# Performance work log

Hardware: AMD Instinct MI355X
Metric: run time of the kernel (lower is better)

The kernel has to match this reference:

```python
import jax, jax.numpy as jnp
import numpy as np

IOU_THRESHOLD = 0.5
ROIS_NUMBER = 256


def setup_inputs() -> dict:
    key = jax.random.key(0)
    k1, k2, k3 = jax.random.split(key, 3)
    B, N = 8, 4096
    scores = jax.random.uniform(k1, (B, N, 1), dtype=jnp.float32)
    xy = jax.random.uniform(k2, (B, N, 2), dtype=jnp.float32) * 100.0
    wh = jax.random.uniform(k3, (B, N, 2), dtype=jnp.float32) * 20.0 + 1.0
    return {"input": jnp.concatenate([scores, xy, wh], axis=-1)}


def _make_corners(regs):
    # regs: [N,4] = (x, y, w, h); TF uses floor-div by 2 (`//`) on floats
    x, y, w, h = regs[:, 0], regs[:, 1], regs[:, 2], regs[:, 3]
    ws = w // 2
    hs = h // 2
    return jnp.stack([x - ws, y - hs, x + ws, y + hs], axis=-1)


def _nms_single(preds, key):
    # preds: [N,5] = (score, x, y, w, h)
    N = preds.shape[0]
    scores = preds[:, 0]
    boxes = _make_corners(preds[:, 1:])
    order = jnp.argsort(-scores)                       # descending score
    b = boxes[order]
    x1, y1, x2, y2 = b[:, 0], b[:, 1], b[:, 2], b[:, 3]
    area = (x2 - x1) * (y2 - y1)
    # pairwise IoU [N,N] (selection only -> stop_gradient)
    ix1 = jnp.maximum(x1[:, None], x1[None, :])
    iy1 = jnp.maximum(y1[:, None], y1[None, :])
    ix2 = jnp.minimum(x2[:, None], x2[None, :])
    iy2 = jnp.minimum(y2[:, None], y2[None, :])
    inter = jnp.maximum(ix2 - ix1, 0.0) * jnp.maximum(iy2 - iy1, 0.0)
    union = area[:, None] + area[None, :] - inter
    iou = jax.lax.stop_gradient(jnp.where(union > 0, inter / union, 0.0))

    idx = jnp.arange(N)

    def step(suppressed, i):
        keep_i = ~suppressed[i]
        suppressed = suppressed | (keep_i & (iou[i] > IOU_THRESHOLD) & (idx > i))
        return suppressed, keep_i

    _, keep = jax.lax.scan(step, jnp.zeros((N,), bool), idx)

    # first ROIS_NUMBER kept positions (in score order); N marks "not kept"
    pos = jnp.sort(jnp.where(keep, idx, N))[:ROIS_NUMBER]
    valid = pos < N
    sel = order[jnp.minimum(pos, N - 1)]
    rand_idx = jax.random.randint(key, (ROIS_NUMBER,), 0, N)
    sel = jnp.where(valid, sel, rand_idx)              # pad with random regions
    return preds[sel][:, 1:]                           # [ROIS,4] = (x,y,w,h)


def reference(input) -> jnp.ndarray:
    B = input.shape[0]
    keys = jax.random.split(jax.random.key(42), B)
    return jax.vmap(_nms_single)(input, keys)
```

## Files before the change

### kernel.cpp

```cpp
#include <hip/hip_runtime.h>
#include <stdint.h>

#pragma clang fp contract(off)

#define NMS_B 8
#define NMS_N 4096
#define ROIS 256
#define SEL_TAU 0.85f

typedef unsigned long long u64;
typedef unsigned int u32;

__device__ __forceinline__ int lds_slot(int e) { return e + (e >> 2); }

__device__ __forceinline__ u64 rdlane_u64(u64 v, int l) {
    u32 lo = (u32)__builtin_amdgcn_readlane((int)(u32)v, l);
    u32 hi = (u32)__builtin_amdgcn_readlane((int)(u32)(v >> 32), l);
    return ((u64)hi << 32) | lo;
}

__device__ __forceinline__ bool sup_pred(float4 rc, float rh, float4 cc, float ch) {
    float iw = fmaxf(fminf(rc.z, cc.z) - fmaxf(rc.x, cc.x), 0.0f);
    float ih = fmaxf(fminf(rc.w, cc.w) - fmaxf(rc.y, cc.y), 0.0f);
    float inter = iw * ih;
    return inter > fmaf(-0.5f, inter, rh + ch);
}


__global__ __launch_bounds__(1024, 1) void nms_k1(
        const float* __restrict__ in, float4* __restrict__ crn512,
        float* __restrict__ ha512, u32* __restrict__ sidx512,
        int* __restrict__ flag) {
    __shared__ u64 sm[3584];
    __shared__ int s_selCount;
    const int b = blockIdx.x, t = threadIdx.x;
    const int lane = t & 63;
    const size_t base = (size_t)b * NMS_N;

    u64* selKey = sm;
    u64* sortA0 = sm + 1024;
    u64* sortA1 = sm + 2304;

    float sc[4];
    #pragma unroll
    for (int r = 0; r < 4; ++r) {
        int e = t + 1024 * r;
        sc[r] = in[(base + e) * 5];
    }
    if (t == 0) s_selCount = 0;
    __syncthreads();

    #pragma unroll
    for (int r = 0; r < 4; ++r) {
        bool pred = (sc[r] >= SEL_TAU);
        u64 m = __ballot(pred);
        u32 cnt = (u32)__popcll(m);
        int wbase = 0;
        if (lane == 0 && cnt) wbase = atomicAdd(&s_selCount, (int)cnt);
        wbase = __shfl(wbase, 0, 64);
        if (pred) {
            int slot = wbase + (int)__popcll(m & ((1ULL << lane) - 1ULL));
            if (slot < 1024) {
                int e = t + 1024 * r;
                selKey[slot] = ((u64)(~__float_as_uint(sc[r])) << 32) | (u32)e;
            }
        }
    }
    __syncthreads();
    const int selCount = s_selCount;
    const bool fullPath = (selCount < 512) || (selCount > 1024);
    if (t == 0) flag[b] = fullPath ? 1 : 0;
    if (fullPath) return;

    u64 kk = (t < selCount) ? selKey[t] : ~0ULL;
    int s = 0;
    for (int k = 2; k <= 1024; k <<= 1) {
        int j = k >> 1;
        for (; j >= 64; j >>= 1) {
            u64* buf = s ? sortA1 : sortA0;
            buf[lds_slot(t)] = kk;
            __syncthreads();
            u64 part = buf[lds_slot(t ^ j)];
            bool up = ((t & k) == 0), lower = ((t & j) == 0);
            u64 mn = kk < part ? kk : part, mx = kk < part ? part : kk;
            kk = (up == lower) ? mn : mx;
            s ^= 1;
        }
        for (; j >= 1; j >>= 1) {
            u64 part = __shfl_xor(kk, j, 64);
            bool up = ((t & k) == 0), lower = ((t & j) == 0);
            u64 mn = kk < part ? kk : part, mx = kk < part ? part : kk;
            kk = (up == lower) ? mn : mx;
        }
    }

    if (t < 512) {
        u32 orig = (u32)kk;
        const float* bp = in + (base + orig) * 5;
        float x = bp[1], y = bp[2], w = bp[3], h = bp[4];
        float ws_ = floorf(w * 0.5f), hs_ = floorf(h * 0.5f);
        float4 c4 = make_float4(x - ws_, y - hs_, x + ws_, y + hs_);
        size_t g = (size_t)b * 512 + t;
        crn512[g] = c4;
        ha512[g] = 0.5f * ((c4.z - c4.x) * (c4.w - c4.y));
        sidx512[g] = orig;
    }
}

__global__ __launch_bounds__(256, 1) void nms_k2(
        const float4* __restrict__ crn512, const float* __restrict__ ha512,
        const int* __restrict__ flag, u64* __restrict__ hbuf) {
    const int b = blockIdx.y, blk = blockIdx.x;
    if (flag[b]) return;
    __shared__ float4 crn_s[512];
    __shared__ float  ha_s[512];
    const int t = threadIdx.x, lane = t & 63, wid = t >> 6;

    for (int i = t; i < 512; i += 256) {
        crn_s[i] = crn512[(size_t)b * 512 + i];
        ha_s[i]  = ha512[(size_t)b * 512 + i];
    }
    __syncthreads();

    u32* h32 = (u32*)hbuf;
    #pragma unroll
    for (int s = 0; s < 2; ++s) {
        int tau = blk * 8 + wid * 2 + s;
        int u = tau >> 1, hf = tau & 1;
        int kr = 0;
        while ((kr + 1) * (kr + 2) / 2 <= u) ++kr;
        int w = u - kr * (kr + 1) / 2;
        float4 myc = crn_s[64 * kr + lane];
        float  myh = ha_s[64 * kr + lane];
        u32 word = 0;
        const int q0 = hf * 32;
        #pragma unroll 8
        for (int q = 0; q < 32; ++q) {
            bool p = sup_pred(crn_s[64 * w + q0 + q], ha_s[64 * w + q0 + q], myc, myh);
            word |= (u32)(p ? 1u : 0u) << q;
        }
        h32[(((size_t)b * 36 + u) * 64 + lane) * 2 + hf] = word;
    }
}

__global__ __launch_bounds__(1024, 1) void nms_k3(
        const float* __restrict__ in, const u32* __restrict__ sidx512,
        const u64* __restrict__ hbuf, const int* __restrict__ flag,
        u32* __restrict__ sortedIdx, float4* __restrict__ crn,
        float* __restrict__ ha, float* __restrict__ outp) {
    __shared__ u64 sm[5120];
    __shared__ int kept[ROIS];
    __shared__ int s_need;
    const int b = blockIdx.x, t = threadIdx.x;
    const int lane = t & 63, wid = t >> 6;
    const size_t base = (size_t)b * NMS_N;

    int flg = flag[b];
    if (!flg) {
        for (int i = t; i < 2304; i += 1024) sm[i] = hbuf[(size_t)b * 2304 + i];
        for (int r = t; r < ROIS; r += 1024) kept[r] = 0;
        if (t == 0) s_need = 0;
        __syncthreads();

        if (t < 64) {
            u64* h_lds = sm;
            int count = 0;
            u32 f[8];
            #pragma unroll
            for (int k = 0; k < 8; ++k) f[k] = 1u;
            bool done = false;
            #pragma unroll
            for (int g = 0; g < 8; ++g) {
                if (!done) {
                    u64 hgg = h_lds[(g * (g + 1) / 2 + g) * 64 + lane];
                    u64 kb = 0;
                    u64 avail = __ballot(f[g] != 0);
                    while (avail != 0 && count < ROIS) {
                        int r = __builtin_ctzll(avail);
                        if (lane == 0) kept[count] = g * 64 + r;
                        ++count;
                        kb |= 1ULL << r;
                        u64 w = rdlane_u64(hgg, r);
                        avail &= ~(w | (1ULL << r));
                    }
                    if (count >= ROIS) {
                        done = true;
                    } else {
                        #pragma unroll
                        for (int k2 = g + 1; k2 < 8; ++k2)
                            f[k2] &= (u32)((h_lds[(k2 * (k2 + 1) / 2 + g) * 64 + lane] & kb) == 0);
                    }
                }
            }
            if (t == 0) s_need = (count >= ROIS) ? 0 : 1;
        }
        __syncthreads();
        flg = s_need;
    }

    if (flg) {
        u64 key[4];
        #pragma unroll
        for (int r = 0; r < 4; ++r) {
            int e = 4 * t + r;
            float s = in[(base + e) * 5];
            key[r] = ((u64)(~__float_as_uint(s)) << 32) | (u32)e;
        }
        for (int k = 2; k <= 4096; k <<= 1) {
            int j = k >> 1;
            if (j >= 256) {
                #pragma unroll
                for (int r = 0; r < 4; ++r) sm[lds_slot(4 * t + r)] = key[r];
                __syncthreads();
                for (; j >= 256; j >>= 1) {
                    for (int el = t; el < 4096; el += 1024) {
                        int p = el ^ j;
                        if (p > el) {
                            u64 a = sm[lds_slot(el)], cc = sm[lds_slot(p)];
                            bool up = ((el & k) == 0);
                            if ((a > cc) == up) { sm[lds_slot(el)] = cc; sm[lds_slot(p)] = a; }
                        }
                    }
                    __syncthreads();
                }
                #pragma unroll
                for (int r = 0; r < 4; ++r) key[r] = sm[lds_slot(4 * t + r)];
            }
            for (; j >= 4; j >>= 1) {
                int d = j >> 2;
                #pragma unroll
                for (int r = 0; r < 4; ++r) {
                    int e = 4 * t + r;
                    u64 mine = key[r];
                    u64 part = __shfl_xor(mine, d, 64);
                    bool up = ((e & k) == 0);
                    bool lower = ((e & j) == 0);
                    u64 mn = (mine < part) ? mine : part;
                    u64 mx = (mine < part) ? part : mine;
                    key[r] = (up == lower) ? mn : mx;
                }
            }
            for (; j >= 1; j >>= 1) {
                #pragma unroll
                for (int r = 0; r < 4; ++r) {
                    int pr = r | j;
                    if (((r & j) == 0) && pr < 4) {
                        int e = 4 * t + r;
                        bool up = ((e & k) == 0);
                        u64 a = key[r], cc = key[pr];
                        if ((a > cc) == up) { key[r] = cc; key[pr] = a; }
                    }
                }
            }
        }
        __syncthreads();

        u64*    h2 = sm;
        float4* crn2 = (float4*)(sm + 2304);
        float*  ha2  = (float*)(sm + 2304 + 1024);

        #pragma unroll
        for (int r = 0; r < 4; ++r) {
            int e = 4 * t + r;
            u32 orig = (u32)key[r];
            const float* bp = in + (base + orig) * 5;
            float x = bp[1], y = bp[2], w = bp[3], h = bp[4];
            float ws_ = floorf(w * 0.5f), hs_ = floorf(h * 0.5f);
            float4 c4 = make_float4(x - ws_, y - hs_, x + ws_, y + hs_);
            float hv = 0.5f * ((c4.z - c4.x) * (c4.w - c4.y));
            size_t g = base + e;
            sortedIdx[g] = orig;
            crn[g] = c4;
            ha[g] = hv;
            if (e < 512) { crn2[e] = c4; ha2[e] = hv; }
        }
        for (int r = t; r < ROIS; r += 1024) kept[r] = 0;
        __syncthreads();

        for (int u = wid; u < 36; u += 16) {
            int kr = 0;
            while ((kr + 1) * (kr + 2) / 2 <= u) ++kr;
            int w = u - kr * (kr + 1) / 2;
            float4 myc = crn2[64 * kr + lane];
            float  myh = ha2[64 * kr + lane];
            u64 word = 0;
            #pragma unroll 4
            for (int q = 0; q < 64; ++q) {
                bool p = sup_pred(crn2[64 * w + q], ha2[64 * w + q], myc, myh);
                word |= ((u64)(p ? 1u : 0u)) << q;
            }
            h2[(size_t)u * 64 + lane] = word;
        }
        __syncthreads();

        if (t < 64) {
            int count = 0;
            u32 f[8];
            #pragma unroll
            for (int k = 0; k < 8; ++k) f[k] = 1u;
            bool done = false;
            #pragma unroll
            for (int g = 0; g < 8; ++g) {
                if (!done) {
                    u64 hgg = h2[(size_t)(g * (g + 1) / 2 + g) * 64 + lane];
                    u64 kb = 0;
                    u64 avail = __ballot(f[g] != 0);
                    while (avail != 0 && count < ROIS) {
                        int r = __builtin_ctzll(avail);
                        if (lane == 0) kept[count] = g * 64 + r;
                        ++count;
                        kb |= 1ULL << r;
                        u32 bit = (u32)(hgg >> r) & 1u;
                        f[g] &= (bit ^ 1u) & (u32)(lane != r);
                        avail = __ballot(f[g] != 0);
                    }
                    if (count >= ROIS) {
                        done = true;
                    } else {
                        #pragma unroll
                        for (int k2 = g + 1; k2 < 8; ++k2)
                            f[k2] &= (u32)((h2[(size_t)(k2 * (k2 + 1) / 2 + g) * 64 + lane] & kb) == 0);
                    }
                }
            }
            if (count < ROIS) {
                for (int Wp = 4; Wp < 32 && count < ROIS; ++Wp) {
                    const int cLo = 128 * Wp + lane, cHi = cLo + 64;
                    float4 cL = crn[base + cLo]; float hL = ha[base + cLo];
                    float4 cH = crn[base + cHi]; float hH = ha[base + cHi];
                    u32 fLo = 1u, fHi = 1u;
                    for (int j2 = 0; j2 < count; ++j2) {
                        int pos = kept[j2];
                        float4 kc = crn[base + pos]; float kh = ha[base + pos];
                        fLo &= (u32)(!sup_pred(kc, kh, cL, hL));
                        fHi &= (u32)(!sup_pred(kc, kh, cH, hH));
                    }
                    u64 curLo0 = 0, curHi0 = 0, curHi1 = 0;
                    for (int r = 0; r < 64; ++r) {
                        float4 rc = crn[base + 128 * Wp + r]; float rh = ha[base + 128 * Wp + r];
                        curLo0 |= ((u64)(sup_pred(rc, rh, cL, hL) ? 1u : 0u)) << r;
                        curHi0 |= ((u64)(sup_pred(rc, rh, cH, hH) ? 1u : 0u)) << r;
                    }
                    for (int r = 0; r < 64; ++r) {
                        float4 rc = crn[base + 128 * Wp + 64 + r]; float rh = ha[base + 128 * Wp + 64 + r];
                        curHi1 |= ((u64)(sup_pred(rc, rh, cH, hH) ? 1u : 0u)) << r;
                    }
                    u64 availLo = __ballot(fLo != 0);
                    while (availLo != 0 && count < ROIS) {
                        int r = __builtin_ctzll(availLo);
                        if (lane == 0) kept[count] = Wp * 128 + r;
                        ++count;
                        fLo &= (u32)(((curLo0 >> r) & 1ULL) ^ 1ULL) & (u32)(lane != r);
                        fHi &= (u32)(((curHi0 >> r) & 1ULL) ^ 1ULL);
                        availLo = __ballot(fLo != 0);
                    }
                    u64 availHi = __ballot(fHi != 0);
                    while (availHi != 0 && count < ROIS) {
                        int r = __builtin_ctzll(availHi);
                        if (lane == 0) kept[count] = Wp * 128 + 64 + r;
                        ++count;
                        fHi &= (u32)(((curHi1 >> r) & 1ULL) ^ 1ULL) & (u32)(lane != r);
                        availHi = __ballot(fHi != 0);
                    }
                }
            }
        }
    }
    __syncthreads();

    if (t < ROIS) {
        int pos = kept[t];
        int orig = flg ? (int)sortedIdx[base + pos]
                       : (int)sidx512[(size_t)b * 512 + pos];
        const float* bp = in + (base + orig) * 5;
        ((float4*)outp)[(size_t)b * ROIS + t] =
            make_float4(bp[1], bp[2], bp[3], bp[4]);
    }
}

extern "C" void kernel_launch(void* const* d_in, const int* in_sizes, int n_in,
                              void* d_out, int out_size, void* d_ws, size_t ws_size,
                              hipStream_t stream) {
    const float* in = (const float*)d_in[0];
    float* out = (float*)d_out;
    char* ws = (char*)d_ws;

    u32* sortedIdx = (u32*)ws;                  size_t off = (size_t)NMS_B * NMS_N * 4;
    float4* crn = (float4*)(ws + off);          off += (size_t)NMS_B * NMS_N * 16;
    float* ha = (float*)(ws + off);             off += (size_t)NMS_B * NMS_N * 4;
    float4* crn512 = (float4*)(ws + off);       off += (size_t)NMS_B * 512 * 16;
    float* ha512 = (float*)(ws + off);          off += (size_t)NMS_B * 512 * 4;
    u32* sidx512 = (u32*)(ws + off);            off += (size_t)NMS_B * 512 * 4;
    u64* hbuf = (u64*)(ws + off);               off += (size_t)NMS_B * 36 * 64 * 8;
    int* flag = (int*)(ws + off);               off += NMS_B * 4;

    nms_k1<<<NMS_B, 1024, 0, stream>>>(in, crn512, ha512, sidx512, flag);
    nms_k2<<<dim3(9, NMS_B), 256, 0, stream>>>(crn512, ha512, flag, hbuf);
    nms_k3<<<NMS_B, 1024, 0, stream>>>(in, sidx512, hbuf, flag, sortedIdx, crn, ha, out);
}
```

Before: 92.95 us.

## Move fast-path greedy scan into k2 via last-block atomic, full path into k1

The full-sort fallback path moves into k1. The fast-path greedy selection and output write move from k3 into k2, where the last-arriving block per batch (atomic counter with threadfences) runs the scan. k2 now launches twice as many blocks, each doing one word, and writes kept indices by popcount instead of serially. k3 becomes a rarely-taken recovery path gated by needFull. This removes the separate 1024-thread k3 pass and its hbuf reload on the common path, at the cost of atomic/fence overhead and duplicated code.

```diff
diff --git a/kernel.cpp b/kernel.cpp
--- a/kernel.cpp
+++ b/kernel.cpp
@@ -30,11 +30,14 @@
 __global__ __launch_bounds__(1024, 1) void nms_k1(
         const float* __restrict__ in, float4* __restrict__ crn512,
         float* __restrict__ ha512, u32* __restrict__ sidx512,
-        int* __restrict__ flag) {
-    __shared__ u64 sm[3584];
+        int* __restrict__ flag, int* __restrict__ done, int* __restrict__ needFull,
+        u32* __restrict__ sortedIdx, float4* __restrict__ crn,
+        float* __restrict__ ha, float* __restrict__ outp) {
+    __shared__ u64 sm[5120];
+    __shared__ int kept[ROIS];
     __shared__ int s_selCount;
     const int b = blockIdx.x, t = threadIdx.x;
-    const int lane = t & 63;
+    const int lane = t & 63, wid = t >> 6;
     const size_t base = (size_t)b * NMS_N;
 
     u64* selKey = sm;
@@ -47,7 +50,7 @@
         int e = t + 1024 * r;
         sc[r] = in[(base + e) * 5];
     }
-    if (t == 0) s_selCount = 0;
+    if (t == 0) { s_selCount = 0; done[b] = 0; needFull[b] = 0; }
     __syncthreads();
 
     #pragma unroll
@@ -70,135 +73,44 @@
     const int selCount = s_selCount;
     const bool fullPath = (selCount < 512) || (selCount > 1024);
     if (t == 0) flag[b] = fullPath ? 1 : 0;
-    if (fullPath) return;
-
-    u64 kk = (t < selCount) ? selKey[t] : ~0ULL;
-    int s = 0;
-    for (int k = 2; k <= 1024; k <<= 1) {
-        int j = k >> 1;
-        for (; j >= 64; j >>= 1) {
-            u64* buf = s ? sortA1 : sortA0;
-            buf[lds_slot(t)] = kk;
-            __syncthreads();
-            u64 part = buf[lds_slot(t ^ j)];
-            bool up = ((t & k) == 0), lower = ((t & j) == 0);
-            u64 mn = kk < part ? kk : part, mx = kk < part ? part : kk;
-            kk = (up == lower) ? mn : mx;
-            s ^= 1;
-        }
-        for (; j >= 1; j >>= 1) {
-            u64 part = __shfl_xor(kk, j, 64);
-            bool up = ((t & k) == 0), lower = ((t & j) == 0);
-            u64 mn = kk < part ? kk : part, mx = kk < part ? part : kk;
-            kk = (up == lower) ? mn : mx;
-        }
-    }
-
-    if (t < 512) {
-        u32 orig = (u32)kk;
-        const float* bp = in + (base + orig) * 5;
-        float x = bp[1], y = bp[2], w = bp[3], h = bp[4];
-        float ws_ = floorf(w * 0.5f), hs_ = floorf(h * 0.5f);
-        float4 c4 = make_float4(x - ws_, y - hs_, x + ws_, y + hs_);
-        size_t g = (size_t)b * 512 + t;
-        crn512[g] = c4;
-        ha512[g] = 0.5f * ((c4.z - c4.x) * (c4.w - c4.y));
-        sidx512[g] = orig;
-    }
-}
-
-__global__ __launch_bounds__(256, 1) void nms_k2(
-        const float4* __restrict__ crn512, const float* __restrict__ ha512,
-        const int* __restrict__ flag, u64* __restrict__ hbuf) {
-    const int b = blockIdx.y, blk = blockIdx.x;
-    if (flag[b]) return;
-    __shared__ float4 crn_s[512];
-    __shared__ float  ha_s[512];
-    const int t = threadIdx.x, lane = t & 63, wid = t >> 6;
-
-    for (int i = t; i < 512; i += 256) {
-        crn_s[i] = crn512[(size_t)b * 512 + i];
-        ha_s[i]  = ha512[(size_t)b * 512 + i];
-    }
-    __syncthreads();
-
-    u32* h32 = (u32*)hbuf;
-    #pragma unroll
-    for (int s = 0; s < 2; ++s) {
-        int tau = blk * 8 + wid * 2 + s;
-        int u = tau >> 1, hf = tau & 1;
-        int kr = 0;
-        while ((kr + 1) * (kr + 2) / 2 <= u) ++kr;
-        int w = u - kr * (kr + 1) / 2;
-        float4 myc = crn_s[64 * kr + lane];
-        float  myh = ha_s[64 * kr + lane];
-        u32 word = 0;
-        const int q0 = hf * 32;
-        #pragma unroll 8
-        for (int q = 0; q < 32; ++q) {
-            bool p = sup_pred(crn_s[64 * w + q0 + q], ha_s[64 * w + q0 + q], myc, myh);
-            word |= (u32)(p ? 1u : 0u) << q;
-        }
-        h32[(((size_t)b * 36 + u) * 64 + lane) * 2 + hf] = word;
-    }
-}
-
-__global__ __launch_bounds__(1024, 1) void nms_k3(
-        const float* __restrict__ in, const u32* __restrict__ sidx512,
-        const u64* __restrict__ hbuf, const int* __restrict__ flag,
-        u32* __restrict__ sortedIdx, float4* __restrict__ crn,
-        float* __restrict__ ha, float* __restrict__ outp) {
-    __shared__ u64 sm[5120];
-    __shared__ int kept[ROIS];
-    __shared__ int s_need;
-    const int b = blockIdx.x, t = threadIdx.x;
-    const int lane = t & 63, wid = t >> 6;
-    const size_t base = (size_t)b * NMS_N;
-
-    int flg = flag[b];
-    if (!flg) {
-        for (int i = t; i < 2304; i += 1024) sm[i] = hbuf[(size_t)b * 2304 + i];
-        for (int r = t; r < ROIS; r += 1024) kept[r] = 0;
-        if (t == 0) s_need = 0;
-        __syncthreads();
-
-        if (t < 64) {
-            u64* h_lds = sm;
-            int count = 0;
-            u32 f[8];
-            #pragma unroll
-            for (int k = 0; k < 8; ++k) f[k] = 1u;
-            bool done = false;
-            #pragma unroll
-            for (int g = 0; g < 8; ++g) {
-                if (!done) {
-                    u64 hgg = h_lds[(g * (g + 1) / 2 + g) * 64 + lane];
-                    u64 kb = 0;
-                    u64 avail = __ballot(f[g] != 0);
-                    while (avail != 0 && count < ROIS) {
-                        int r = __builtin_ctzll(avail);
-                        if (lane == 0) kept[count] = g * 64 + r;
-                        ++count;
-                        kb |= 1ULL << r;
-                        u64 w = rdlane_u64(hgg, r);
-                        avail &= ~(w | (1ULL << r));
-                    }
-                    if (count >= ROIS) {
-                        done = true;
-                    } else {
-                        #pragma unroll
-                        for (int k2 = g + 1; k2 < 8; ++k2)
-                            f[k2] &= (u32)((h_lds[(k2 * (k2 + 1) / 2 + g) * 64 + lane] & kb) == 0);
-                    }
-                }
-            }
-            if (t == 0) s_need = (count >= ROIS) ? 0 : 1;
-        }
-        __syncthreads();
-        flg = s_need;
-    }
-
-    if (flg) {
+
+    if (!fullPath) {
+        u64 kk = (t < selCount) ? selKey[t] : ~0ULL;
+        int s = 0;
+        for (int k = 2; k <= 1024; k <<= 1) {
+            int j = k >> 1;
+            for (; j >= 64; j >>= 1) {
+                u64* buf = s ? sortA1 : sortA0;
+                buf[lds_slot(t)] = kk;
+                __syncthreads();
+                u64 part = buf[lds_slot(t ^ j)];
+                bool up = ((t & k) == 0), lower = ((t & j) == 0);
+                u64 mn = kk < part ? kk : part, mx = kk < part ? part : kk;
+                kk = (up == lower) ? mn : mx;
+                s ^= 1;
+            }
+            for (; j >= 1; j >>= 1) {
+                u64 part = __shfl_xor(kk, j, 64);
+                bool up = ((t & k) == 0), lower = ((t & j) == 0);
+                u64 mn = kk < part ? kk : part, mx = kk < part ? part : kk;
+                kk = (up == lower) ? mn : mx;
+            }
+        }
+        if (t < 512) {
+            u32 orig = (u32)kk;
+            const float* bp = in + (base + orig) * 5;
+            float x = bp[1], y = bp[2], w = bp[3], h = bp[4];
+            float ws_ = floorf(w * 0.5f), hs_ = floorf(h * 0.5f);
+            float4 c4 = make_float4(x - ws_, y - hs_, x + ws_, y + hs_);
+            size_t g = (size_t)b * 512 + t;
+            crn512[g] = c4;
+            ha512[g] = 0.5f * ((c4.z - c4.x) * (c4.w - c4.y));
+            sidx512[g] = orig;
+        }
+        return;
+    }
+
+    {
         u64 key[4];
         #pragma unroll
         for (int r = 0; r < 4; ++r) {
@@ -298,10 +210,10 @@
             u32 f[8];
             #pragma unroll
             for (int k = 0; k < 8; ++k) f[k] = 1u;
-            bool done = false;
+            bool done_ = false;
             #pragma unroll
             for (int g = 0; g < 8; ++g) {
-                if (!done) {
+                if (!done_) {
                     u64 hgg = h2[(size_t)(g * (g + 1) / 2 + g) * 64 + lane];
                     u64 kb = 0;
                     u64 avail = __ballot(f[g] != 0);
@@ -315,7 +227,7 @@
                         avail = __ballot(f[g] != 0);
                     }
                     if (count >= ROIS) {
-                        done = true;
+                        done_ = true;
                     } else {
                         #pragma unroll
                         for (int k2 = g + 1; k2 < 8; ++k2)
@@ -365,13 +277,296 @@
                 }
             }
         }
-    }
-    __syncthreads();
+        __syncthreads();
+        if (t < ROIS) {
+            int pos = kept[t];
+            int orig = (int)sortedIdx[base + pos];
+            const float* bp = in + (base + orig) * 5;
+            ((float4*)outp)[(size_t)b * ROIS + t] =
+                make_float4(bp[1], bp[2], bp[3], bp[4]);
+        }
+    }
+}
+
+__global__ __launch_bounds__(256, 1) void nms_k2(
+        const float* __restrict__ in, const float4* __restrict__ crn512,
+        const float* __restrict__ ha512, const u32* __restrict__ sidx512,
+        const int* __restrict__ flag, int* __restrict__ done,
+        int* __restrict__ needFull, u64* __restrict__ hbuf,
+        float* __restrict__ outp) {
+    const int b = blockIdx.y, blk = blockIdx.x;
+    if (flag[b]) return;
+    __shared__ float4 crn_s[512];
+    __shared__ float  ha_s[512];
+    __shared__ u64    h_lds[2304];
+    __shared__ int    kept[ROIS];
+    __shared__ int    s_last, s_need;
+    const int t = threadIdx.x, lane = t & 63, wid = t >> 6;
+
+    for (int i = t; i < 512; i += 256) {
+        crn_s[i] = crn512[(size_t)b * 512 + i];
+        ha_s[i]  = ha512[(size_t)b * 512 + i];
+    }
+    __syncthreads();
+
+    {
+        int tau = blk * 4 + wid;
+        int u = tau >> 1, hf = tau & 1;
+        int kr = 0;
+        while ((kr + 1) * (kr + 2) / 2 <= u) ++kr;
+        int w = u - kr * (kr + 1) / 2;
+        float4 myc = crn_s[64 * kr + lane];
+        float  myh = ha_s[64 * kr + lane];
+        u32 word = 0;
+        const int q0 = hf * 32;
+        #pragma unroll 8
+        for (int q = 0; q < 32; ++q) {
+            bool p = sup_pred(crn_s[64 * w + q0 + q], ha_s[64 * w + q0 + q], myc, myh);
+            word |= (u32)(p ? 1u : 0u) << q;
+        }
+        ((u32*)hbuf)[(((size_t)b * 36 + u) * 64 + lane) * 2 + hf] = word;
+    }
+
+    __threadfence();
+    __syncthreads();
+    if (t == 0) { int old = atomicAdd(&done[b], 1); s_last = (old == 17); }
+    __syncthreads();
+    if (!s_last) return;
+    __threadfence();
+
+    for (int i = t; i < 2304; i += 256) h_lds[i] = hbuf[(size_t)b * 2304 + i];
+    for (int r = t; r < ROIS; r += 256) kept[r] = 0;
+    if (t == 0) s_need = 0;
+    __syncthreads();
+
+    if (t < 64) {
+        int count = 0;
+        u32 f[8];
+        #pragma unroll
+        for (int k = 0; k < 8; ++k) f[k] = 1u;
+        bool done_ = false;
+        #pragma unroll
+        for (int g = 0; g < 8; ++g) {
+            if (!done_) {
+                u64 hgg = h_lds[(g * (g + 1) / 2 + g) * 64 + lane];
+                u64 kb = 0;
+                const int gbase = count;
+                u64 avail = __ballot(f[g] != 0);
+                while (avail != 0 && count < ROIS) {
+                    int r = __builtin_ctzll(avail);
+                    kb |= 1ULL << r;
+                    ++count;
+                    u64 w = rdlane_u64(hgg, r);
+                    avail &= ~(w | (1ULL << r));
+                }
+                if ((kb >> lane) & 1ULL)
+                    kept[gbase + (int)__popcll(kb & ((1ULL << lane) - 1ULL))] = g * 64 + lane;
+                if (count >= ROIS) {
+                    done_ = true;
+                } else {
+                    #pragma unroll
+                    for (int k2 = g + 1; k2 < 8; ++k2)
+                        f[k2] &= (u32)((h_lds[(k2 * (k2 + 1) / 2 + g) * 64 + lane] & kb) == 0);
+                }
+            }
+        }
+        if (t == 0) s_need = (count >= ROIS) ? 0 : 1;
+    }
+    __syncthreads();
+
+    if (s_need) { if (t == 0) needFull[b] = 1; return; }
 
     if (t < ROIS) {
         int pos = kept[t];
-        int orig = flg ? (int)sortedIdx[base + pos]
-                       : (int)sidx512[(size_t)b * 512 + pos];
+        int orig = (int)sidx512[(size_t)b * 512 + pos];
+        const float* bp = in + ((size_t)b * NMS_N + orig) * 5;
+        ((float4*)outp)[(size_t)b * ROIS + t] =
+            make_float4(bp[1], bp[2], bp[3], bp[4]);
+    }
+}
+
+__global__ __launch_bounds__(1024, 1) void nms_k3(
+        const float* __restrict__ in, const int* __restrict__ needFull,
+        u32* __restrict__ sortedIdx, float4* __restrict__ crn,
+        float* __restrict__ ha, float* __restrict__ outp) {
+    __shared__ u64 sm[5120];
+    __shared__ int kept[ROIS];
+    const int b = blockIdx.x, t = threadIdx.x;
+    const int lane = t & 63, wid = t >> 6;
+    const size_t base = (size_t)b * NMS_N;
+    if (!needFull[b]) return;
+
+    u64 key[4];
+    #pragma unroll
+    for (int r = 0; r < 4; ++r) {
+        int e = 4 * t + r;
+        float s = in[(base + e) * 5];
+        key[r] = ((u64)(~__float_as_uint(s)) << 32) | (u32)e;
+    }
+    for (int k = 2; k <= 4096; k <<= 1) {
+        int j = k >> 1;
+        if (j >= 256) {
+            #pragma unroll
+            for (int r = 0; r < 4; ++r) sm[lds_slot(4 * t + r)] = key[r];
+            __syncthreads();
+            for (; j >= 256; j >>= 1) {
+                for (int el = t; el < 4096; el += 1024) {
+                    int p = el ^ j;
+                    if (p > el) {
+                        u64 a = sm[lds_slot(el)], cc = sm[lds_slot(p)];
+                        bool up = ((el & k) == 0);
+                        if ((a > cc) == up) { sm[lds_slot(el)] = cc; sm[lds_slot(p)] = a; }
+                    }
+                }
+                __syncthreads();
+            }
+            #pragma unroll
+            for (int r = 0; r < 4; ++r) key[r] = sm[lds_slot(4 * t + r)];
+        }
+        for (; j >= 4; j >>= 1) {
+            int d = j >> 2;
+            #pragma unroll
+            for (int r = 0; r < 4; ++r) {
+                int e = 4 * t + r;
+                u64 mine = key[r];
+                u64 part = __shfl_xor(mine, d, 64);
+                bool up = ((e & k) == 0);
+                bool lower = ((e & j) == 0);
+                u64 mn = (mine < part) ? mine : part;
+                u64 mx = (mine < part) ? part : mine;
+                key[r] = (up == lower) ? mn : mx;
+            }
+        }
+        for (; j >= 1; j >>= 1) {
+            #pragma unroll
+            for (int r = 0; r < 4; ++r) {
+                int pr = r | j;
+                if (((r & j) == 0) && pr < 4) {
+                    int e = 4 * t + r;
+                    bool up = ((e & k) == 0);
+                    u64 a = key[r], cc = key[pr];
+                    if ((a > cc) == up) { key[r] = cc; key[pr] = a; }
+                }
+            }
+        }
+    }
+    __syncthreads();
+
+    u64*    h2 = sm;
+    float4* crn2 = (float4*)(sm + 2304);
+    float*  ha2  = (float*)(sm + 2304 + 1024);
+
+    #pragma unroll
+    for (int r = 0; r < 4; ++r) {
+        int e = 4 * t + r;
+        u32 orig = (u32)key[r];
+        const float* bp = in + (base + orig) * 5;
+        float x = bp[1], y = bp[2], w = bp[3], h = bp[4];
+        float ws_ = floorf(w * 0.5f), hs_ = floorf(h * 0.5f);
+        float4 c4 = make_float4(x - ws_, y - hs_, x + ws_, y + hs_);
+        float hv = 0.5f * ((c4.z - c4.x) * (c4.w - c4.y));
+        size_t g = base + e;
+        sortedIdx[g] = orig;
+        crn[g] = c4;
+        ha[g] = hv;
+        if (e < 512) { crn2[e] = c4; ha2[e] = hv; }
+    }
+    for (int r = t; r < ROIS; r += 1024) kept[r] = 0;
+    __syncthreads();
+
+    for (int u = wid; u < 36; u += 16) {
+        int kr = 0;
+        while ((kr + 1) * (kr + 2) / 2 <= u) ++kr;
+        int w = u - kr * (kr + 1) / 2;
+        float4 myc = crn2[64 * kr + lane];
+        float  myh = ha2[64 * kr + lane];
+        u64 word = 0;
+        #pragma unroll 4
+        for (int q = 0; q < 64; ++q) {
+            bool p = sup_pred(crn2[64 * w + q], ha2[64 * w + q], myc, myh);
+            word |= ((u64)(p ? 1u : 0u)) << q;
+        }
+        h2[(size_t)u * 64 + lane] = word;
+    }
+    __syncthreads();
+
+    if (t < 64) {
+        int count = 0;
+        u32 f[8];
+        #pragma unroll
+        for (int k = 0; k < 8; ++k) f[k] = 1u;
+        bool done_ = false;
+        #pragma unroll
+        for (int g = 0; g < 8; ++g) {
+            if (!done_) {
+                u64 hgg = h2[(size_t)(g * (g + 1) / 2 + g) * 64 + lane];
+                u64 kb = 0;
+                u64 avail = __ballot(f[g] != 0);
+                while (avail != 0 && count < ROIS) {
+                    int r = __builtin_ctzll(avail);
+                    if (lane == 0) kept[count] = g * 64 + r;
+                    ++count;
+                    kb |= 1ULL << r;
+                    u32 bit = (u32)(hgg >> r) & 1u;
+                    f[g] &= (bit ^ 1u) & (u32)(lane != r);
+                    avail = __ballot(f[g] != 0);
+                }
+                if (count >= ROIS) {
+                    done_ = true;
+                } else {
+                    #pragma unroll
+                    for (int k2 = g + 1; k2 < 8; ++k2)
+                        f[k2] &= (u32)((h2[(size_t)(k2 * (k2 + 1) / 2 + g) * 64 + lane] & kb) == 0);
+                }
+            }
+        }
+        if (count < ROIS) {
+            for (int Wp = 4; Wp < 32 && count < ROIS; ++Wp) {
+                const int cLo = 128 * Wp + lane, cHi = cLo + 64;
+                float4 cL = crn[base + cLo]; float hL = ha[base + cLo];
+                float4 cH = crn[base + cHi]; float hH = ha[base + cHi];
+                u32 fLo = 1u, fHi = 1u;
+                for (int j2 = 0; j2 < count; ++j2) {
+                    int pos = kept[j2];
+                    float4 kc = crn[base + pos]; float kh = ha[base + pos];
+                    fLo &= (u32)(!sup_pred(kc, kh, cL, hL));
+                    fHi &= (u32)(!sup_pred(kc, kh, cH, hH));
+                }
+                u64 curLo0 = 0, curHi0 = 0, curHi1 = 0;
+                for (int r = 0; r < 64; ++r) {
+                    float4 rc = crn[base + 128 * Wp + r]; float rh = ha[base + 128 * Wp + r];
+                    curLo0 |= ((u64)(sup_pred(rc, rh, cL, hL) ? 1u : 0u)) << r;
+                    curHi0 |= ((u64)(sup_pred(rc, rh, cH, hH) ? 1u : 0u)) << r;
+                }
+                for (int r = 0; r < 64; ++r) {
+                    float4 rc = crn[base + 128 * Wp + 64 + r]; float rh = ha[base + 128 * Wp + 64 + r];
+                    curHi1 |= ((u64)(sup_pred(rc, rh, cH, hH) ? 1u : 0u)) << r;
+                }
+                u64 availLo = __ballot(fLo != 0);
+                while (availLo != 0 && count < ROIS) {
+                    int r = __builtin_ctzll(availLo);
+                    if (lane == 0) kept[count] = Wp * 128 + r;
+                    ++count;
+                    fLo &= (u32)(((curLo0 >> r) & 1ULL) ^ 1ULL) & (u32)(lane != r);
+                    fHi &= (u32)(((curHi0 >> r) & 1ULL) ^ 1ULL);
+                    availLo = __ballot(fLo != 0);
+                }
+                u64 availHi = __ballot(fHi != 0);
+                while (availHi != 0 && count < ROIS) {
+                    int r = __builtin_ctzll(availHi);
+                    if (lane == 0) kept[count] = Wp * 128 + 64 + r;
+                    ++count;
+                    fHi &= (u32)(((curHi1 >> r) & 1ULL) ^ 1ULL) & (u32)(lane != r);
+                    availHi = __ballot(fHi != 0);
+                }
+            }
+        }
+    }
+    __syncthreads();
+
+    if (t < ROIS) {
+        int pos = kept[t];
+        int orig = (int)sortedIdx[base + pos];
         const float* bp = in + (base + orig) * 5;
         ((float4*)outp)[(size_t)b * ROIS + t] =
             make_float4(bp[1], bp[2], bp[3], bp[4]);
@@ -393,8 +588,12 @@
     u32* sidx512 = (u32*)(ws + off);            off += (size_t)NMS_B * 512 * 4;
     u64* hbuf = (u64*)(ws + off);               off += (size_t)NMS_B * 36 * 64 * 8;
     int* flag = (int*)(ws + off);               off += NMS_B * 4;
-
-    nms_k1<<<NMS_B, 1024, 0, stream>>>(in, crn512, ha512, sidx512, flag);
-    nms_k2<<<dim3(9, NMS_B), 256, 0, stream>>>(crn512, ha512, flag, hbuf);
-    nms_k3<<<NMS_B, 1024, 0, stream>>>(in, sidx512, hbuf, flag, sortedIdx, crn, ha, out);
+    int* done = (int*)(ws + off);               off += NMS_B * 4;
+    int* needFull = (int*)(ws + off);           off += NMS_B * 4;
+
+    nms_k1<<<NMS_B, 1024, 0, stream>>>(in, crn512, ha512, sidx512, flag, done,
+                                       needFull, sortedIdx, crn, ha, out);
+    nms_k2<<<dim3(18, NMS_B), 256, 0, stream>>>(in, crn512, ha512, sidx512,
+                                                flag, done, needFull, hbuf, out);
+    nms_k3<<<NMS_B, 1024, 0, stream>>>(in, needFull, sortedIdx, crn, ha, out);
 }
```

Result: slower. 98.45 us (+5.9%).
